# Performance work log

Measured on AMD Instinct MI355X. Metric: run time of the kernel, lower is better.

Reference implementation:

```python
import jax, jax.numpy as jnp
import numpy as np

B = 8
SEQ = 8192
D_MODEL = 256
D_STATE = 64
D_CONV = 4
EXPAND = 4
HEADDIM = 64
N_LAYERS = 8
D_INNER = EXPAND * D_MODEL            # 1024
NHEADS = D_INNER // HEADDIM           # 16
CONV_DIM = D_INNER + 2 * D_STATE      # 1152 (ngroups=1)
D_IN_PROJ = 2 * D_INNER + 2 * D_STATE + NHEADS  # 2192


def setup_inputs():
    key = jax.random.key(0)
    ks = jax.random.split(key, 16)
    rn = lambda k, shape, fan: jax.random.normal(k, shape, jnp.float32) / np.float32(np.sqrt(fan))
    inp = {}
    inp["x"] = jax.random.normal(ks[0], (B, 3, SEQ), jnp.float32)
    inp["conv1_w"] = rn(ks[1], (64, 3, 16), 3 * 16)
    inp["conv1_b"] = rn(ks[2], (64,), 64)
    inp["conv2_w"] = rn(ks[3], (D_MODEL, 64, 16), 64 * 16)
    inp["conv2_b"] = rn(ks[4], (D_MODEL,), D_MODEL)
    inp["in_proj_w"] = rn(ks[5], (N_LAYERS, D_IN_PROJ, D_MODEL), D_MODEL)
    inp["dw_conv_w"] = rn(ks[6], (N_LAYERS, CONV_DIM, D_CONV), D_CONV)
    inp["dw_conv_b"] = rn(ks[7], (N_LAYERS, CONV_DIM), D_CONV)
    inp["dt_bias"] = jax.random.normal(ks[8], (N_LAYERS, NHEADS), jnp.float32) * 0.5
    inp["A_log"] = jax.random.uniform(ks[9], (N_LAYERS, NHEADS), jnp.float32, 0.0, 2.0)
    inp["ssm_D"] = jnp.ones((N_LAYERS, NHEADS), jnp.float32)
    inp["rms_w"] = jnp.ones((N_LAYERS, D_INNER), jnp.float32)
    inp["out_proj_w"] = rn(ks[10], (N_LAYERS, D_MODEL, D_INNER), D_INNER)
    inp["ln_w"] = jnp.ones((D_MODEL,), jnp.float32)
    inp["ln_b"] = jnp.zeros((D_MODEL,), jnp.float32)
    inp["reg1_w"] = rn(ks[11], (128, D_MODEL), D_MODEL)
    inp["reg1_b"] = rn(ks[12], (128,), 128)
    inp["reg2_w"] = rn(ks[13], (1, 128), 128)
    inp["reg2_b"] = rn(ks[14], (1,), 128)
    return inp


def _silu(v):
    return v * jax.nn.sigmoid(v)


def _mamba2_layer(u, in_proj_w, dw_w, dw_b, dt_bias, A_log, ssm_D, rms_w, out_proj_w):
    b, l, _ = u.shape
    zxbcdt = u @ in_proj_w.T                               # (b,l,2192)
    z = zxbcdt[..., :D_INNER]
    xBC = zxbcdt[..., D_INNER:D_INNER + CONV_DIM]
    dt = jax.nn.softplus(zxbcdt[..., D_INNER + CONV_DIM:] + dt_bias)   # (b,l,h)
    # causal depthwise conv1d (kernel D_CONV), then SiLU
    pad = jnp.pad(xBC, ((0, 0), (D_CONV - 1, 0), (0, 0)))
    conv = sum(pad[:, k:k + l, :] * dw_w[:, k] for k in range(D_CONV)) + dw_b
    xBC = _silu(conv)
    xh = xBC[..., :D_INNER].reshape(b, l, NHEADS, HEADDIM)  # (b,l,h,p)
    Bm = xBC[..., D_INNER:D_INNER + D_STATE]                # (b,l,n)
    Cm = xBC[..., D_INNER + D_STATE:]                       # (b,l,n)
    dA = jnp.exp(dt * (-jnp.exp(A_log)))                    # (b,l,h)

    def step(h, inp):
        dA_t, dt_t, x_t, B_t, C_t = inp
        h = h * dA_t[:, :, None, None] + (dt_t[:, :, None] * x_t)[..., None] * B_t[:, None, None, :]
        y = jnp.einsum('bhpn,bn->bhp', h, C_t)
        return h, y

    h0 = jnp.zeros((b, NHEADS, HEADDIM, D_STATE), u.dtype)
    xs = (dA.transpose(1, 0, 2), dt.transpose(1, 0, 2),
          xh.transpose(1, 0, 2, 3), Bm.transpose(1, 0, 2), Cm.transpose(1, 0, 2))
    _, ys = jax.lax.scan(step, h0, xs)                      # (l,b,h,p)
    y = ys.transpose(1, 0, 2, 3) + ssm_D[None, None, :, None] * xh
    y = y.reshape(b, l, D_INNER)
    y = y * _silu(z)                                        # gated
    y = y * jax.lax.rsqrt(jnp.mean(y * y, axis=-1, keepdims=True) + 1e-5) * rms_w
    return y @ out_proj_w.T


def reference(x, conv1_w, conv1_b, conv2_w, conv2_b, in_proj_w, dw_conv_w, dw_conv_b,
              dt_bias, A_log, ssm_D, rms_w, out_proj_w, ln_w, ln_b,
              reg1_w, reg1_b, reg2_w, reg2_b):
    dn = ('NCH', 'OIH', 'NCH')
    h = jax.lax.conv_general_dilated(x, conv1_w, (4,), [(6, 6)], dimension_numbers=dn) + conv1_b[None, :, None]
    h = jax.nn.gelu(h, approximate=False)
    h = jax.lax.conv_general_dilated(h, conv2_w, (2,), [(7, 7)], dimension_numbers=dn) + conv2_b[None, :, None]
    h = jax.nn.gelu(h, approximate=False)
    h = h.transpose(0, 2, 1)                                # (b, 1024, d_model)
    for i in range(N_LAYERS):
        h = _mamba2_layer(h, in_proj_w[i], dw_conv_w[i], dw_conv_b[i],
                          dt_bias[i], A_log[i], ssm_D[i], rms_w[i], out_proj_w[i])
    mu = jnp.mean(h, -1, keepdims=True)
    var = jnp.mean((h - mu) ** 2, -1, keepdims=True)
    h = (h - mu) * jax.lax.rsqrt(var + 1e-5) * ln_w + ln_b  # LayerNorm
    pooled = h.mean(1)
    r = jax.nn.gelu(pooled @ reg1_w.T + reg1_b, approximate=False)
    return r @ reg2_w.T + reg2_b                            # (b, 1)
```

## Files before the change

kernel.cpp:

```cpp
#include <hip/hip_runtime.h>
#include <math.h>

#define NB       8
#define SEQ      8192
#define L1OUT    2048
#define LOUT     1024
#define DMODEL   256
#define DINNER   1024
#define NHEADS   16
#define HEADDIM  64
#define DSTATE   64
#define CONVDIM  1152
#define DINPROJ  2192
#define NPADIN   2304
#define NLAYERS  8
#define NCHUNK   16
#define Q        64

typedef _Float16 f16;
typedef __attribute__((ext_vector_type(8))) _Float16 f16x8;
typedef __attribute__((ext_vector_type(4))) _Float16 f16x4;
typedef __attribute__((ext_vector_type(4))) float    f32x4;

__device__ __forceinline__ float gelu_f(float v) {
    return 0.5f * v * (1.0f + erff(v * 0.70710678118654752f));
}
__device__ __forceinline__ float silu_f(float v) {
    return v * __builtin_amdgcn_rcpf(1.0f + __expf(-v));
}

__device__ __forceinline__ void gload16(const void* g, void* l) {
    __builtin_amdgcn_global_load_lds(
        (const __attribute__((address_space(1))) unsigned int*)g,
        (__attribute__((address_space(3))) unsigned int*)l, 16, 0, 0);
}

__global__ __launch_bounds__(256) void k_cast(const float* __restrict__ in,
                                              f16* __restrict__ out, int n) {
    int i = blockIdx.x * 256 + threadIdx.x;
    if (i < n) out[i] = (f16)in[i];
}

__global__ __launch_bounds__(256) void k_cast_inproj(const float* __restrict__ w,
                                                     f16* __restrict__ out) {
    int idx = blockIdx.x * 256 + threadIdx.x;
    int c = idx & 255;
    int r = (idx >> 8) % NPADIN;
    int l = idx / (NPADIN * 256);
    float v = (r < DINPROJ) ? w[((size_t)l * DINPROJ + r) * 256 + c] : 0.f;
    out[idx] = (f16)v;
}

__global__ __launch_bounds__(256) void k_conv1(const float* __restrict__ x,
                                               const float* __restrict__ w,
                                               const float* __restrict__ bias,
                                               f16* __restrict__ out) {
    int idx = blockIdx.x * 256 + threadIdx.x;
    int t  = idx & (L1OUT - 1);
    int co = (idx >> 11) & 63;
    int b  = idx >> 17;
    float s = bias[co];
#pragma unroll
    for (int ci = 0; ci < 3; ++ci) {
        const float* xp = x + ((size_t)b * 3 + ci) * SEQ;
        const float* wp = w + (co * 3 + ci) * 16;
#pragma unroll
        for (int k = 0; k < 16; ++k) {
            int pos = t * 4 + k - 6;
            if (pos >= 0 && pos < SEQ) s = fmaf(xp[pos], wp[k], s);
        }
    }
    out[idx] = (f16)gelu_f(s);
}

__global__ __launch_bounds__(256) void k_im2col(const f16* __restrict__ h1,
                                                f16* __restrict__ A) {
    int idx = blockIdx.x * 256 + threadIdx.x;
    int col = idx & 1023;
    int row = idx >> 10;
    int t = row & (LOUT - 1);
    int b = row >> 10;
    int ci = col >> 4, k = col & 15;
    int pos = t * 2 + k - 7;
    f16 v = (f16)0.f;
    if (pos >= 0 && pos < L1OUT) v = h1[((size_t)b * 64 + ci) * L1OUT + pos];
    A[idx] = v;
}

template<int BM, int EPI>
__global__ __launch_bounds__(256) void k_hgemm(const f16* __restrict__ A,
                                               const f16* __restrict__ Bw,
                                               f16* __restrict__ Ch,
                                               int M, int N, int K,
                                               const float* __restrict__ bias,
                                               const float* __restrict__ dt_bias,
                                               const float* __restrict__ A_log,
                                               float* __restrict__ dadt) {
    constexpr int MI = BM / 32;
    __shared__ f16 As[BM * 32];
    __shared__ f16 Bs[128 * 32];
    int tid  = threadIdx.x;
    int lane = tid & 63, wid = tid >> 6;
    int wm = wid >> 1, wn = wid & 1;
    int row0 = blockIdx.y * BM, col0 = blockIdx.x * 128;
    int lr = lane & 15, kb = lane >> 4;

    f32x4 acc[MI][4];
#pragma unroll
    for (int mi = 0; mi < MI; ++mi)
#pragma unroll
        for (int ni = 0; ni < 4; ++ni)
            acc[mi][ni] = (f32x4){0.f, 0.f, 0.f, 0.f};

    int srow = tid >> 2;
    int scol = (tid & 3) * 8;

    for (int k0 = 0; k0 < K; k0 += 32) {
        __syncthreads();
#pragma unroll
        for (int is = 0; is < BM / 64; ++is)
            gload16(A + (size_t)(row0 + is * 64 + srow) * K + k0 + scol,
                    &As[is * 2048 + wid * 512]);
#pragma unroll
        for (int is = 0; is < 2; ++is)
            gload16(Bw + (size_t)(col0 + is * 64 + srow) * K + k0 + scol,
                    &Bs[is * 2048 + wid * 512]);
        __syncthreads();

        f16x8 a[MI], b[4];
#pragma unroll
        for (int mi = 0; mi < MI; ++mi)
            a[mi] = *reinterpret_cast<const f16x8*>(
                &As[(wm * (BM / 2) + mi * 16 + lr) * 32 + kb * 8]);
#pragma unroll
        for (int ni = 0; ni < 4; ++ni)
            b[ni] = *reinterpret_cast<const f16x8*>(
                &Bs[(wn * 64 + ni * 16 + lr) * 32 + kb * 8]);
#pragma unroll
        for (int mi = 0; mi < MI; ++mi)
#pragma unroll
            for (int ni = 0; ni < 4; ++ni)
                acc[mi][ni] = __builtin_amdgcn_mfma_f32_16x16x32_f16(
                    a[mi], b[ni], acc[mi][ni], 0, 0, 0);
    }

#pragma unroll
    for (int mi = 0; mi < MI; ++mi)
#pragma unroll
        for (int ni = 0; ni < 4; ++ni) {
            int ccol = col0 + wn * 64 + ni * 16 + lr;
            if (ccol < N) {
                int rbase = row0 + wm * (BM / 2) + mi * 16 + kb * 4;
                f32x4 v = acc[mi][ni];
#pragma unroll
                for (int r = 0; r < 4; ++r) {
                    float val = v[r];
                    if (EPI == 1) val = gelu_f(val + bias[ccol]);
                    Ch[(size_t)(rbase + r) * N + ccol] = (f16)val;
                    if (EPI == 2 && ccol >= DINNER + CONVDIM) {
                        int hh = ccol - (DINNER + CONVDIM);
                        float raw = val + dt_bias[hh];
                        float dtv = (raw > 20.f) ? raw : log1pf(__expf(raw));
                        float lda = -__expf(A_log[hh]) * dtv;
                        *(float2*)&dadt[(size_t)(rbase + r) * 32 + hh * 2] =
                            make_float2(lda, dtv);
                    }
                }
            }
        }
}

__global__ __launch_bounds__(256) void k_ssd1(const f16* __restrict__ zx16,
                                              const float* __restrict__ dadt,
                                              const float* __restrict__ dw_w,
                                              const float* __restrict__ dw_b,
                                              const float* __restrict__ ssmD,
                                              f16* __restrict__ y1,
                                              f16* __restrict__ Sbuf16,
                                              float* __restrict__ Abuf,
                                              f16* __restrict__ C16) {
    __shared__ f16 Bs[64][72];
    __shared__ f16 Cs[64][72];
    __shared__ float GT[64][68];
    __shared__ f16 Mw[4][64][72];
    __shared__ float2 LaDt[4][64];

    int tid = threadIdx.x, lane = tid & 63, wid = tid >> 6;
    int bid = blockIdx.x;
    int hq = bid & 3, c = (bid >> 2) & 15, b = bid >> 6;
    int h = hq * 4 + wid;
    int lr = lane & 15, kb = lane >> 4;
    f16* Xs = &Mw[0][0][0];

    {
        int sg = tid % 48;
        int ts = tid / 48;
        if (ts < 4) {
            int xc;
            if (sg < 32)      xc = hq * 256 + sg * 8;
            else if (sg < 40) xc = 1024 + (sg - 32) * 8;
            else              xc = 1088 + (sg - 40) * 8;
            int zc = 1024 + xc;
            float4 wv[8];
            float  bv[8];
#pragma unroll
            for (int j = 0; j < 8; ++j) {
                wv[j] = *(const float4*)&dw_w[(xc + j) * 4];
                bv[j] = dw_b[xc + j];
            }
            int l0 = c * 64 + ts * 16;
            const f16* zrow = zx16 + ((size_t)(b * 1024 + l0)) * DINPROJ + zc;
            f16x8 r0, r1, r2, r3;
            f16x8 zz;
#pragma unroll
            for (int j = 0; j < 8; ++j) zz[j] = (f16)0.f;
            r0 = (l0 >= 3) ? *(const f16x8*)(zrow - 3 * DINPROJ) : zz;
            r1 = (l0 >= 2) ? *(const f16x8*)(zrow - 2 * DINPROJ) : zz;
            r2 = (l0 >= 1) ? *(const f16x8*)(zrow - 1 * DINPROJ) : zz;
#pragma unroll
            for (int t = 0; t < 16; ++t) {
                r3 = *(const f16x8*)(zrow + t * DINPROJ);
                f16x8 o;
#pragma unroll
                for (int j = 0; j < 8; ++j) {
                    float s = bv[j];
                    s = fmaf((float)r0[j], wv[j].x, s);
                    s = fmaf((float)r1[j], wv[j].y, s);
                    s = fmaf((float)r2[j], wv[j].z, s);
                    s = fmaf((float)r3[j], wv[j].w, s);
                    o[j] = (f16)silu_f(s);
                }
                int row = ts * 16 + t;
                if (sg < 32) {
                    f16x4 o0 = {o[0], o[1], o[2], o[3]};
                    f16x4 o1 = {o[4], o[5], o[6], o[7]};
                    *(f16x4*)&Xs[row * 260 + sg * 8]     = o0;
                    *(f16x4*)&Xs[row * 260 + sg * 8 + 4] = o1;
                } else if (sg < 40) {
                    *(f16x8*)&Bs[row][(sg - 32) * 8] = o;
                } else {
                    *(f16x8*)&Cs[row][(sg - 40) * 8] = o;
                }
                r0 = r1; r1 = r2; r2 = r3;
            }
        }
    }

    float2 ad = *(const float2*)&dadt[((size_t)(b * 1024 + c * 64 + lane) * 16 + h) * 2];
    float La = ad.x;
#pragma unroll
    for (int o = 1; o < 64; o <<= 1) {
        float v = __shfl_up(La, o);
        if (lane >= o) La += v;
    }
    float dt_own = ad.y;
    float La63 = __shfl(La, 63);
    float w_own = __expf(La63 - La) * dt_own;
    LaDt[wid][lane] = make_float2(La, dt_own);
    float Dh = ssmD[h];
    __syncthreads();

    if (hq == 0) {
        f16* cp = C16 + (((size_t)(b * 16 + c)) << 12);
#pragma unroll
        for (int it = 0; it < 2; ++it) {
            int cid = it * 256 + tid;
            int row = cid >> 3, off = (cid & 7) * 8;
            *(f16x8*)&cp[row * 64 + off] = *(const f16x8*)&Cs[row][off];
        }
    }

    f16x8 xfrag[4][2];
#pragma unroll
    for (int pi = 0; pi < 4; ++pi)
#pragma unroll
        for (int ks = 0; ks < 2; ++ks) {
            f16x8 v;
#pragma unroll
            for (int j = 0; j < 8; ++j)
                v[j] = Xs[(ks * 32 + kb * 8 + j) * 260 + wid * 64 + pi * 16 + lr];
            xfrag[pi][ks] = v;
        }

    {
        int tq = wid & 1, sq = wid >> 1;
        f32x4 g[2][2];
#pragma unroll
        for (int i = 0; i < 2; ++i)
#pragma unroll
            for (int j = 0; j < 2; ++j) g[i][j] = (f32x4){0.f, 0.f, 0.f, 0.f};
#pragma unroll
        for (int ks = 0; ks < 2; ++ks) {
            f16x8 a[2], bb[2];
#pragma unroll
            for (int ti = 0; ti < 2; ++ti)
                a[ti] = *(const f16x8*)&Cs[tq * 32 + ti * 16 + lr][ks * 32 + kb * 8];
#pragma unroll
            for (int si = 0; si < 2; ++si)
                bb[si] = *(const f16x8*)&Bs[sq * 32 + si * 16 + lr][ks * 32 + kb * 8];
#pragma unroll
            for (int ti = 0; ti < 2; ++ti)
#pragma unroll
                for (int si = 0; si < 2; ++si)
                    g[ti][si] = __builtin_amdgcn_mfma_f32_16x16x32_f16(
                        a[ti], bb[si], g[ti][si], 0, 0, 0);
        }
#pragma unroll
        for (int ti = 0; ti < 2; ++ti)
#pragma unroll
            for (int si = 0; si < 2; ++si)
#pragma unroll
                for (int r = 0; r < 4; ++r)
                    GT[sq * 32 + si * 16 + lr][tq * 32 + ti * 16 + kb * 4 + r] = g[ti][si][r];
    }
    __syncthreads();

    {
        f16x8 brow[8];
#pragma unroll
        for (int i = 0; i < 8; ++i) brow[i] = *(const f16x8*)&Bs[lane][i * 8];
#pragma unroll
        for (int i = 0; i < 8; ++i)
#pragma unroll
            for (int j = 0; j < 8; ++j)
                Mw[wid][i * 8 + j][lane] = (f16)((float)brow[i][j] * w_own);
    }
    __builtin_amdgcn_wave_barrier();

    f16x8 sbfrag[4][2];
#pragma unroll
    for (int ni = 0; ni < 4; ++ni)
#pragma unroll
        for (int ks = 0; ks < 2; ++ks)
            sbfrag[ni][ks] = *(const f16x8*)&Mw[wid][ni * 16 + lr][ks * 32 + kb * 8];

    {
        f32x4 accS[4][4];
#pragma unroll
        for (int pi = 0; pi < 4; ++pi)
#pragma unroll
            for (int ni = 0; ni < 4; ++ni) accS[pi][ni] = (f32x4){0.f, 0.f, 0.f, 0.f};
#pragma unroll
        for (int ks = 0; ks < 2; ++ks)
#pragma unroll
            for (int pi = 0; pi < 4; ++pi)
#pragma unroll
                for (int ni = 0; ni < 4; ++ni)
                    accS[pi][ni] = __builtin_amdgcn_mfma_f32_16x16x32_f16(
                        xfrag[pi][ks], sbfrag[ni][ks], accS[pi][ni], 0, 0, 0);
        size_t sbase = ((size_t)((b * 16 + h) * 16 + c)) << 12;
#pragma unroll
        for (int pi = 0; pi < 4; ++pi)
#pragma unroll
            for (int ni = 0; ni < 4; ++ni)
#pragma unroll
                for (int r = 0; r < 4; ++r)
                    Sbuf16[sbase + (size_t)(pi * 16 + kb * 4 + r) * 64 + ni * 16 + lr] =
                        (f16)accS[pi][ni][r];
        if (lane == 0) Abuf[(b * 16 + h) * 16 + c] = __expf(La63);
    }
    __builtin_amdgcn_wave_barrier();

    {
        int t = lane;
        float la_t = La;
#pragma unroll
        for (int s8 = 0; s8 < 8; ++s8) {
            f16x8 mv;
#pragma unroll
            for (int j = 0; j < 8; ++j) {
                int s = s8 * 8 + j;
                float2 ld = LaDt[wid][s];
                float m = (s <= t) ? GT[s][t] * __expf(la_t - ld.x) * ld.y : 0.f;
                if (s == t) m += Dh;
                mv[j] = (f16)m;
            }
            *(f16x8*)&Mw[wid][t][s8 * 8] = mv;
        }
    }
    __builtin_amdgcn_wave_barrier();

    {
        f32x4 accY[4][4];
#pragma unroll
        for (int ti = 0; ti < 4; ++ti)
#pragma unroll
            for (int pi = 0; pi < 4; ++pi) accY[ti][pi] = (f32x4){0.f, 0.f, 0.f, 0.f};
#pragma unroll
        for (int ks = 0; ks < 2; ++ks) {
            f16x8 af[4];
#pragma unroll
            for (int ti = 0; ti < 4; ++ti)
                af[ti] = *(const f16x8*)&Mw[wid][ti * 16 + lr][ks * 32 + kb * 8];
#pragma unroll
            for (int ti = 0; ti < 4; ++ti)
#pragma unroll
                for (int pi = 0; pi < 4; ++pi)
                    accY[ti][pi] = __builtin_amdgcn_mfma_f32_16x16x32_f16(
                        af[ti], xfrag[pi][ks], accY[ti][pi], 0, 0, 0);
        }
        f16* yp = y1 + ((size_t)(b * 1024 + c * 64)) * 1024 + h * 64;
#pragma unroll
        for (int ti = 0; ti < 4; ++ti)
#pragma unroll
            for (int pi = 0; pi < 4; ++pi)
#pragma unroll
                for (int r = 0; r < 4; ++r)
                    yp[(size_t)(ti * 16 + kb * 4 + r) * 1024 + pi * 16 + lr] =
                        (f16)accY[ti][pi][r];
    }
}

__global__ __launch_bounds__(64) void k_hscan(const f16* __restrict__ Sbuf16,
                                              const float* __restrict__ Abuf,
                                              f16* __restrict__ H16) {
    int tid = threadIdx.x;
    int bid = blockIdx.x;
    int bh = bid >> 2, q = bid & 3;
    size_t base = (size_t)bh << 16;
    int off = q * 1024 + tid * 16;
    float Hl[16];
#pragma unroll
    for (int j = 0; j < 16; ++j) Hl[j] = 0.f;
    for (int c = 0; c < NCHUNK; ++c) {
        f16x8 o0, o1;
#pragma unroll
        for (int j = 0; j < 8; ++j) { o0[j] = (f16)Hl[j]; o1[j] = (f16)Hl[j + 8]; }
        *(f16x8*)&H16[base + (size_t)c * 4096 + off] = o0;
        *(f16x8*)&H16[base + (size_t)c * 4096 + off + 8] = o1;
        float A = Abuf[bh * 16 + c];
        f16x8 s0 = *(const f16x8*)&Sbuf16[base + (size_t)c * 4096 + off];
        f16x8 s1 = *(const f16x8*)&Sbuf16[base + (size_t)c * 4096 + off + 8];
#pragma unroll
        for (int j = 0; j < 8; ++j) {
            Hl[j]     = fmaf(Hl[j],     A, (float)s0[j]);
            Hl[j + 8] = fmaf(Hl[j + 8], A, (float)s1[j]);
        }
    }
}

__global__ __launch_bounds__(64) void k_ssd2(const f16* __restrict__ C16,
                                             const float* __restrict__ dadt,
                                             const f16* __restrict__ H16,
                                             f16* __restrict__ y2) {
    __shared__ float La64[64];
    int lane = threadIdx.x;
    int bid = blockIdx.x;
    int h = bid & 15, c = (bid >> 4) & 15, b = bid >> 8;
    int lr = lane & 15, kb = lane >> 4;

    f16x8 hfrag[4][2];
    const f16* Hh = H16 + (((size_t)((b * 16 + h) * 16 + c)) << 12);
#pragma unroll
    for (int pi = 0; pi < 4; ++pi)
#pragma unroll
        for (int ks = 0; ks < 2; ++ks)
            hfrag[pi][ks] = *(const f16x8*)(Hh + (size_t)(pi * 16 + lr) * 64 + ks * 32 + kb * 8);

    float2 ad = *(const float2*)&dadt[((size_t)(b * 1024 + c * 64 + lane) * 16 + h) * 2];
    float La = ad.x;
#pragma unroll
    for (int o = 1; o < 64; o <<= 1) {
        float v = __shfl_up(La, o);
        if (lane >= o) La += v;
    }
    La64[lane] = La;
    __syncthreads();

    const f16* cp = C16 + (((size_t)(b * 16 + c)) << 12);
    f32x4 acc[4][4];
#pragma unroll
    for (int ti = 0; ti < 4; ++ti)
#pragma unroll
        for (int pi = 0; pi < 4; ++pi) acc[ti][pi] = (f32x4){0.f, 0.f, 0.f, 0.f};
#pragma unroll
    for (int ks = 0; ks < 2; ++ks) {
        f16x8 af[4];
#pragma unroll
        for (int ti = 0; ti < 4; ++ti)
            af[ti] = *(const f16x8*)(cp + (ti * 16 + lr) * 64 + ks * 32 + kb * 8);
#pragma unroll
        for (int ti = 0; ti < 4; ++ti)
#pragma unroll
            for (int pi = 0; pi < 4; ++pi)
                acc[ti][pi] = __builtin_amdgcn_mfma_f32_16x16x32_f16(
                    af[ti], hfrag[pi][ks], acc[ti][pi], 0, 0, 0);
    }
    f16* yp = y2 + ((size_t)(b * 1024 + c * 64)) * 1024 + h * 64;
#pragma unroll
    for (int ti = 0; ti < 4; ++ti)
#pragma unroll
        for (int r = 0; r < 4; ++r) {
            int t = ti * 16 + kb * 4 + r;
            float sc = __expf(La64[t]);
#pragma unroll
            for (int pi = 0; pi < 4; ++pi)
                yp[(size_t)t * 1024 + pi * 16 + lr] = (f16)(sc * acc[ti][pi][r]);
        }
}

__global__ __launch_bounds__(256) void k_gate(const f16* __restrict__ zx16,
                                              const float* __restrict__ rmsw,
                                              const f16* __restrict__ y1,
                                              const f16* __restrict__ y2,
                                              f16* __restrict__ ygate) {
    __shared__ float sh[4];
    int bl = blockIdx.x, tid = threadIdx.x;
    int c = tid * 4;
    f16x4 y1v = *reinterpret_cast<const f16x4*>(&y1[(size_t)bl * DINNER + c]);
    f16x4 y2v = *reinterpret_cast<const f16x4*>(&y2[(size_t)bl * DINNER + c]);
    f16x4 z4  = *reinterpret_cast<const f16x4*>(&zx16[(size_t)bl * DINPROJ + c]);
    float v[4];
    float ss = 0.f;
#pragma unroll
    for (int j = 0; j < 4; ++j) {
        v[j] = ((float)y1v[j] + (float)y2v[j]) * silu_f((float)z4[j]);
        ss += v[j] * v[j];
    }
    int lane = tid & 63, wid = tid >> 6;
#pragma unroll
    for (int o = 32; o > 0; o >>= 1) ss += __shfl_down(ss, o, 64);
    if (lane == 0) sh[wid] = ss;
    __syncthreads();
    float total = sh[0] + sh[1] + sh[2] + sh[3];
    float r = rsqrtf(total * (1.f / DINNER) + 1e-5f);
    f16x4 o4;
    o4.x = (f16)(v[0] * r * rmsw[c + 0]);
    o4.y = (f16)(v[1] * r * rmsw[c + 1]);
    o4.z = (f16)(v[2] * r * rmsw[c + 2]);
    o4.w = (f16)(v[3] * r * rmsw[c + 3]);
    *reinterpret_cast<f16x4*>(&ygate[(size_t)bl * DINNER + c]) = o4;
}

__global__ __launch_bounds__(256) void k_lnpool(const f16* __restrict__ h,
                                                const float* __restrict__ lnw,
                                                const float* __restrict__ lnb,
                                                float* __restrict__ pooled) {
    __shared__ float pl[4][256];
    int bid = blockIdx.x;
    int b = bid >> 5, seg = bid & 31;
    int tid = threadIdx.x, lane = tid & 63, w = tid >> 6;
    int c4 = lane * 4;
    float4 lw = *(const float4*)&lnw[c4];
    float4 lb = *(const float4*)&lnb[c4];
    float acc0 = 0.f, acc1 = 0.f, acc2 = 0.f, acc3 = 0.f;
    const f16* hb = h + ((size_t)b * 1024 + seg * 32 + w * 8) * DMODEL;
#pragma unroll
    for (int i = 0; i < 8; ++i) {
        f16x4 hv = *(const f16x4*)(hb + (size_t)i * DMODEL + c4);
        float vx = (float)hv.x, vy = (float)hv.y, vz = (float)hv.z, vw = (float)hv.w;
        float s1 = vx + vy + vz + vw;
        float s2 = vx * vx + vy * vy + vz * vz + vw * vw;
#pragma unroll
        for (int o = 32; o > 0; o >>= 1) {
            s1 += __shfl_xor(s1, o);
            s2 += __shfl_xor(s2, o);
        }
        float mu = s1 * (1.f / DMODEL);
        float var = s2 * (1.f / DMODEL) - mu * mu;
        float rr = rsqrtf(var + 1e-5f);
        acc0 += (vx - mu) * rr * lw.x + lb.x;
        acc1 += (vy - mu) * rr * lw.y + lb.y;
        acc2 += (vz - mu) * rr * lw.z + lb.z;
        acc3 += (vw - mu) * rr * lw.w + lb.w;
    }
    pl[w][c4 + 0] = acc0; pl[w][c4 + 1] = acc1;
    pl[w][c4 + 2] = acc2; pl[w][c4 + 3] = acc3;
    __syncthreads();
    float tot = pl[0][tid] + pl[1][tid] + pl[2][tid] + pl[3][tid];
    atomicAdd(&pooled[b * DMODEL + tid], tot * (1.f / LOUT));
}

__global__ void k_zero(float* __restrict__ p, int n) {
    int i = blockIdx.x * 256 + threadIdx.x;
    if (i < n) p[i] = 0.f;
}

__global__ __launch_bounds__(128) void k_head(const float* __restrict__ pooled,
                                              const float* __restrict__ w1,
                                              const float* __restrict__ b1,
                                              const float* __restrict__ w2,
                                              const float* __restrict__ b2,
                                              float* __restrict__ out) {
    __shared__ float red[2];
    int b = blockIdx.x, j = threadIdx.x;
    float acc = b1[j];
#pragma unroll 8
    for (int d = 0; d < DMODEL; ++d)
        acc = fmaf(pooled[b * DMODEL + d], w1[j * DMODEL + d], acc);
    float r = gelu_f(acc) * w2[j];
#pragma unroll
    for (int o = 32; o > 0; o >>= 1) r += __shfl_down(r, o, 64);
    int lane = j & 63, wid = j >> 6;
    if (lane == 0) red[wid] = r;
    __syncthreads();
    if (j == 0) out[b] = red[0] + red[1] + b2[0];
}

extern "C" void kernel_launch(void* const* d_in, const int* in_sizes, int n_in,
                              void* d_out, int out_size, void* d_ws, size_t ws_size,
                              hipStream_t stream) {
    const float* x         = (const float*)d_in[0];
    const float* conv1_w   = (const float*)d_in[1];
    const float* conv1_b   = (const float*)d_in[2];
    const float* conv2_w   = (const float*)d_in[3];
    const float* conv2_b   = (const float*)d_in[4];
    const float* in_proj_w = (const float*)d_in[5];
    const float* dw_w      = (const float*)d_in[6];
    const float* dw_b      = (const float*)d_in[7];
    const float* dt_bias   = (const float*)d_in[8];
    const float* A_log     = (const float*)d_in[9];
    const float* ssm_D     = (const float*)d_in[10];
    const float* rms_w     = (const float*)d_in[11];
    const float* out_proj_w= (const float*)d_in[12];
    const float* ln_w      = (const float*)d_in[13];
    const float* ln_b      = (const float*)d_in[14];
    const float* reg1_w    = (const float*)d_in[15];
    const float* reg1_b    = (const float*)d_in[16];
    const float* reg2_w    = (const float*)d_in[17];
    const float* reg2_b    = (const float*)d_in[18];

    float* ws = (float*)d_ws;
    size_t off = 0;
    float* dadt   = ws + off; off += (size_t)NB * LOUT * NHEADS * 2;
    float* Abuf   = ws + off; off += (size_t)NB * NHEADS * NCHUNK;
    float* pooled = ws + off; off += NB * DMODEL;

    f16* fbase = (f16*)(ws + off);
    size_t foff = 0;
    f16* c1f16  = fbase + foff; foff += (size_t)NB * 64 * L1OUT;
    f16* hbf0   = fbase + foff; foff += (size_t)NB * LOUT * DMODEL;
    f16* hbf1   = fbase + foff; foff += (size_t)NB * LOUT * DMODEL;
    f16* ygate  = fbase + foff; foff += (size_t)NB * LOUT * DINNER;
    f16* y2     = fbase + foff; foff += (size_t)NB * LOUT * DINNER;
    f16* y1     = fbase + foff; foff += (size_t)NB * LOUT * DINNER;
    f16* C16    = fbase + foff; foff += (size_t)NB * NCHUNK * 64 * 64;
    f16* zx16   = fbase + foff; foff += (size_t)NB * LOUT * DINPROJ;
    f16* Sbuf16 = fbase + foff; foff += (size_t)NB * NHEADS * NCHUNK * 4096;
    f16* w_in_h = fbase + foff; foff += (size_t)NLAYERS * NPADIN * DMODEL;
    f16* w_out_h= fbase + foff; foff += (size_t)NLAYERS * DMODEL * DINNER;
    f16* w_c2_h = fbase + foff; foff += (size_t)DMODEL * 1024;
    f16* H16    = ygate;
    f16* im2h   = y1;

    k_cast_inproj<<<(NLAYERS * NPADIN * 256) / 256, 256, 0, stream>>>(in_proj_w, w_in_h);
    k_cast<<<(NLAYERS * DMODEL * DINNER) / 256, 256, 0, stream>>>(
        out_proj_w, w_out_h, NLAYERS * DMODEL * DINNER);
    k_cast<<<(DMODEL * 1024) / 256, 256, 0, stream>>>(conv2_w, w_c2_h, DMODEL * 1024);

    k_conv1<<<(NB * 64 * L1OUT) / 256, 256, 0, stream>>>(x, conv1_w, conv1_b, c1f16);
    k_im2col<<<(NB * LOUT * 1024) / 256, 256, 0, stream>>>(c1f16, im2h);
    {
        dim3 g(256 / 128, 8192 / 64);
        k_hgemm<64, 1><<<g, 256, 0, stream>>>(im2h, w_c2_h, hbf0,
                                              8192, 256, 1024, conv2_b,
                                              nullptr, nullptr, nullptr);
    }

    f16* hcur = hbf0;
    f16* hnxt = hbf1;
    for (int i = 0; i < NLAYERS; ++i) {
        {
            dim3 g(NPADIN / 128, 8192 / 128);
            k_hgemm<128, 2><<<g, 256, 0, stream>>>(
                hcur, w_in_h + (size_t)i * NPADIN * DMODEL, zx16,
                8192, DINPROJ, DMODEL, nullptr,
                dt_bias + i * NHEADS, A_log + i * NHEADS, dadt);
        }
        k_ssd1<<<NB * NCHUNK * 4, 256, 0, stream>>>(
            zx16, dadt, dw_w + (size_t)i * CONVDIM * 4, dw_b + (size_t)i * CONVDIM,
            ssm_D + i * NHEADS, y1, Sbuf16, Abuf, C16);
        k_hscan<<<NB * NHEADS * 4, 64, 0, stream>>>(Sbuf16, Abuf, H16);
        k_ssd2<<<NB * NCHUNK * NHEADS, 64, 0, stream>>>(C16, dadt, H16, y2);
        k_gate<<<NB * LOUT, 256, 0, stream>>>(zx16, rms_w + (size_t)i * DINNER,
                                              y1, y2, ygate);
        {
            dim3 g(DMODEL / 128, 8192 / 64);
            k_hgemm<64, 0><<<g, 256, 0, stream>>>(
                ygate, w_out_h + (size_t)i * DMODEL * DINNER, hnxt,
                8192, DMODEL, DINNER, nullptr, nullptr, nullptr, nullptr);
        }
        f16* tmp = hcur; hcur = hnxt; hnxt = tmp;
    }

    k_zero<<<(NB * DMODEL + 255) / 256, 256, 0, stream>>>(pooled, NB * DMODEL);
    k_lnpool<<<NB * 32, 256, 0, stream>>>(hcur, ln_w, ln_b, pooled);
    k_head<<<NB, 128, 0, stream>>>(pooled, reg1_w, reg1_b, reg2_w, reg2_b, (float*)d_out);
}
```

Before: 944.4 us.

## Fuse state scan into SSD output kernel, widen GEMM K-tile, vectorize conv stages

Fuses the inter-chunk state scan with the C·H output matmul, so chunk states stay in LDS instead of going through a global buffer. The GEMM now uses a 64-wide K tile with an XOR-swizzled shared-memory layout to cut bank conflicts and halve the barrier count. conv1 computes 8 outputs per thread from register-cached inputs, and im2col writes 8-wide vectors. The pooled-output atomics and zero kernel are replaced by per-segment partial sums reduced in the head kernel. In exchange, the fused SSD kernel launches only 128 blocks with 128KB of LDS each, which can leave much of the GPU idle.

```diff
diff --git a/kernel.cpp b/kernel.cpp
--- a/kernel.cpp
+++ b/kernel.cpp
@@ -56,35 +56,67 @@
                                                const float* __restrict__ bias,
                                                f16* __restrict__ out) {
     int idx = blockIdx.x * 256 + threadIdx.x;
-    int t  = idx & (L1OUT - 1);
-    int co = (idx >> 11) & 63;
-    int b  = idx >> 17;
-    float s = bias[co];
+    int u  = idx & 255;
+    int co = (idx >> 8) & 63;
+    int b  = idx >> 14;
+    int xbase = u * 32 - 8;
+
+    float acc[8];
+#pragma unroll
+    for (int t = 0; t < 8; ++t) acc[t] = bias[co];
+
 #pragma unroll
     for (int ci = 0; ci < 3; ++ci) {
         const float* xp = x + ((size_t)b * 3 + ci) * SEQ;
+        float xb[48];
+#pragma unroll
+        for (int j = 0; j < 12; ++j) {
+            int off = xbase + j * 4;
+            float4 v;
+            if (off >= 0 && off + 3 < SEQ) {
+                v = *(const float4*)&xp[off];
+            } else {
+                v.x = (off + 0 >= 0 && off + 0 < SEQ) ? xp[off + 0] : 0.f;
+                v.y = (off + 1 >= 0 && off + 1 < SEQ) ? xp[off + 1] : 0.f;
+                v.z = (off + 2 >= 0 && off + 2 < SEQ) ? xp[off + 2] : 0.f;
+                v.w = (off + 3 >= 0 && off + 3 < SEQ) ? xp[off + 3] : 0.f;
+            }
+            xb[j * 4 + 0] = v.x; xb[j * 4 + 1] = v.y;
+            xb[j * 4 + 2] = v.z; xb[j * 4 + 3] = v.w;
+        }
         const float* wp = w + (co * 3 + ci) * 16;
-#pragma unroll
-        for (int k = 0; k < 16; ++k) {
-            int pos = t * 4 + k - 6;
-            if (pos >= 0 && pos < SEQ) s = fmaf(xp[pos], wp[k], s);
-        }
-    }
-    out[idx] = (f16)gelu_f(s);
+        float wv[16];
+#pragma unroll
+        for (int k = 0; k < 16; ++k) wv[k] = wp[k];
+#pragma unroll
+        for (int t = 0; t < 8; ++t)
+#pragma unroll
+            for (int k = 0; k < 16; ++k)
+                acc[t] = fmaf(xb[t * 4 + k + 2], wv[k], acc[t]);
+    }
+    f16x8 o;
+#pragma unroll
+    for (int t = 0; t < 8; ++t) o[t] = (f16)gelu_f(acc[t]);
+    *(f16x8*)&out[((size_t)(b * 64 + co)) * L1OUT + u * 8] = o;
 }
 
 __global__ __launch_bounds__(256) void k_im2col(const f16* __restrict__ h1,
                                                 f16* __restrict__ A) {
     int idx = blockIdx.x * 256 + threadIdx.x;
-    int col = idx & 1023;
-    int row = idx >> 10;
+    int g = idx & 127;
+    int row = idx >> 7;
     int t = row & (LOUT - 1);
     int b = row >> 10;
-    int ci = col >> 4, k = col & 15;
-    int pos = t * 2 + k - 7;
-    f16 v = (f16)0.f;
-    if (pos >= 0 && pos < L1OUT) v = h1[((size_t)b * 64 + ci) * L1OUT + pos];
-    A[idx] = v;
+    int ci = g >> 1, k0 = (g & 1) * 8;
+    int pos0 = t * 2 + k0 - 7;
+    const f16* hp = h1 + ((size_t)(b * 64 + ci)) * L1OUT;
+    f16x8 v;
+#pragma unroll
+    for (int j = 0; j < 8; ++j) {
+        int p = pos0 + j;
+        v[j] = (p >= 0 && p < L1OUT) ? hp[p] : (f16)0.f;
+    }
+    *(f16x8*)&A[(size_t)row * 1024 + g * 8] = v;
 }
 
 template<int BM, int EPI>
@@ -97,8 +129,8 @@
                                                const float* __restrict__ A_log,
                                                float* __restrict__ dadt) {
     constexpr int MI = BM / 32;
-    __shared__ f16 As[BM * 32];
-    __shared__ f16 Bs[128 * 32];
+    __shared__ f16 As[BM * 64];
+    __shared__ f16 Bs[128 * 64];
     int tid  = threadIdx.x;
     int lane = tid & 63, wid = tid >> 6;
     int wm = wid >> 1, wn = wid & 1;
@@ -112,36 +144,41 @@
         for (int ni = 0; ni < 4; ++ni)
             acc[mi][ni] = (f32x4){0.f, 0.f, 0.f, 0.f};
 
-    int srow = tid >> 2;
-    int scol = (tid & 3) * 8;
-
-    for (int k0 = 0; k0 < K; k0 += 32) {
+    int sr  = tid >> 3;
+    int scx = ((tid & 7) ^ (sr & 7)) * 8;
+    int rsw = (lr & 7) * 8;
+
+    for (int k0 = 0; k0 < K; k0 += 64) {
         __syncthreads();
 #pragma unroll
-        for (int is = 0; is < BM / 64; ++is)
-            gload16(A + (size_t)(row0 + is * 64 + srow) * K + k0 + scol,
+        for (int is = 0; is < BM / 32; ++is)
+            gload16(A + (size_t)(row0 + is * 32 + sr) * K + k0 + scx,
                     &As[is * 2048 + wid * 512]);
 #pragma unroll
-        for (int is = 0; is < 2; ++is)
-            gload16(Bw + (size_t)(col0 + is * 64 + srow) * K + k0 + scol,
+        for (int is = 0; is < 4; ++is)
+            gload16(Bw + (size_t)(col0 + is * 32 + sr) * K + k0 + scx,
                     &Bs[is * 2048 + wid * 512]);
         __syncthreads();
 
-        f16x8 a[MI], b[4];
-#pragma unroll
-        for (int mi = 0; mi < MI; ++mi)
-            a[mi] = *reinterpret_cast<const f16x8*>(
-                &As[(wm * (BM / 2) + mi * 16 + lr) * 32 + kb * 8]);
-#pragma unroll
-        for (int ni = 0; ni < 4; ++ni)
-            b[ni] = *reinterpret_cast<const f16x8*>(
-                &Bs[(wn * 64 + ni * 16 + lr) * 32 + kb * 8]);
-#pragma unroll
-        for (int mi = 0; mi < MI; ++mi)
+#pragma unroll
+        for (int ks = 0; ks < 2; ++ks) {
+            int cbase = (ks * 32 + kb * 8) ^ rsw;
+            f16x8 a[MI], b[4];
+#pragma unroll
+            for (int mi = 0; mi < MI; ++mi)
+                a[mi] = *reinterpret_cast<const f16x8*>(
+                    &As[(wm * (BM / 2) + mi * 16 + lr) * 64 + cbase]);
 #pragma unroll
             for (int ni = 0; ni < 4; ++ni)
-                acc[mi][ni] = __builtin_amdgcn_mfma_f32_16x16x32_f16(
-                    a[mi], b[ni], acc[mi][ni], 0, 0, 0);
+                b[ni] = *reinterpret_cast<const f16x8*>(
+                    &Bs[(wn * 64 + ni * 16 + lr) * 64 + cbase]);
+#pragma unroll
+            for (int mi = 0; mi < MI; ++mi)
+#pragma unroll
+                for (int ni = 0; ni < 4; ++ni)
+                    acc[mi][ni] = __builtin_amdgcn_mfma_f32_16x16x32_f16(
+                        a[mi], b[ni], acc[mi][ni], 0, 0, 0);
+        }
     }
 
 #pragma unroll
@@ -411,92 +448,100 @@
     }
 }
 
-__global__ __launch_bounds__(64) void k_hscan(const f16* __restrict__ Sbuf16,
-                                              const float* __restrict__ Abuf,
-                                              f16* __restrict__ H16) {
-    int tid = threadIdx.x;
-    int bid = blockIdx.x;
-    int bh = bid >> 2, q = bid & 3;
+__global__ __launch_bounds__(256) void k_ssd2f(const f16* __restrict__ C16,
+                                               const f16* __restrict__ Sbuf16,
+                                               const float* __restrict__ Abuf,
+                                               const float* __restrict__ dadt,
+                                               f16* __restrict__ y2) {
+    __shared__ f16 Hs[NCHUNK][4096];
+    int tid = threadIdx.x, lane = tid & 63, wv = tid >> 6;
+    int bh = blockIdx.x;
+    int h = bh & 15, b = bh >> 4;
+    int lr = lane & 15, kb = lane >> 4;
     size_t base = (size_t)bh << 16;
-    int off = q * 1024 + tid * 16;
-    float Hl[16];
-#pragma unroll
-    for (int j = 0; j < 16; ++j) Hl[j] = 0.f;
-    for (int c = 0; c < NCHUNK; ++c) {
-        f16x8 o0, o1;
-#pragma unroll
-        for (int j = 0; j < 8; ++j) { o0[j] = (f16)Hl[j]; o1[j] = (f16)Hl[j + 8]; }
-        *(f16x8*)&H16[base + (size_t)c * 4096 + off] = o0;
-        *(f16x8*)&H16[base + (size_t)c * 4096 + off + 8] = o1;
-        float A = Abuf[bh * 16 + c];
-        f16x8 s0 = *(const f16x8*)&Sbuf16[base + (size_t)c * 4096 + off];
-        f16x8 s1 = *(const f16x8*)&Sbuf16[base + (size_t)c * 4096 + off + 8];
-#pragma unroll
-        for (int j = 0; j < 8; ++j) {
-            Hl[j]     = fmaf(Hl[j],     A, (float)s0[j]);
-            Hl[j + 8] = fmaf(Hl[j + 8], A, (float)s1[j]);
-        }
-    }
-}
-
-__global__ __launch_bounds__(64) void k_ssd2(const f16* __restrict__ C16,
-                                             const float* __restrict__ dadt,
-                                             const f16* __restrict__ H16,
-                                             f16* __restrict__ y2) {
-    __shared__ float La64[64];
-    int lane = threadIdx.x;
-    int bid = blockIdx.x;
-    int h = bid & 15, c = (bid >> 4) & 15, b = bid >> 8;
-    int lr = lane & 15, kb = lane >> 4;
-
-    f16x8 hfrag[4][2];
-    const f16* Hh = H16 + (((size_t)((b * 16 + h) * 16 + c)) << 12);
-#pragma unroll
-    for (int pi = 0; pi < 4; ++pi)
-#pragma unroll
-        for (int ks = 0; ks < 2; ++ks)
-            hfrag[pi][ks] = *(const f16x8*)(Hh + (size_t)(pi * 16 + lr) * 64 + ks * 32 + kb * 8);
-
-    float2 ad = *(const float2*)&dadt[((size_t)(b * 1024 + c * 64 + lane) * 16 + h) * 2];
-    float La = ad.x;
-#pragma unroll
-    for (int o = 1; o < 64; o <<= 1) {
-        float v = __shfl_up(La, o);
-        if (lane >= o) La += v;
-    }
-    La64[lane] = La;
+
+    {
+        int off = tid * 16;
+        int row = tid >> 2;
+        int c0f = (tid & 3) * 16;
+        int sw = (row & 7) * 8;
+        int d0 = row * 64 + (c0f ^ sw);
+        int d1 = row * 64 + ((c0f + 8) ^ sw);
+        float Hl[16];
+#pragma unroll
+        for (int j = 0; j < 16; ++j) Hl[j] = 0.f;
+#pragma unroll
+        for (int c = 0; c < NCHUNK; ++c) {
+            f16x8 o0, o1;
+#pragma unroll
+            for (int j = 0; j < 8; ++j) { o0[j] = (f16)Hl[j]; o1[j] = (f16)Hl[j + 8]; }
+            *(f16x8*)&Hs[c][d0] = o0;
+            *(f16x8*)&Hs[c][d1] = o1;
+            float A = Abuf[bh * 16 + c];
+            f16x8 s0 = *(const f16x8*)&Sbuf16[base + (size_t)c * 4096 + off];
+            f16x8 s1 = *(const f16x8*)&Sbuf16[base + (size_t)c * 4096 + off + 8];
+#pragma unroll
+            for (int j = 0; j < 8; ++j) {
+                Hl[j]     = fmaf(Hl[j],     A, (float)s0[j]);
+                Hl[j + 8] = fmaf(Hl[j + 8], A, (float)s1[j]);
+            }
+        }
+    }
     __syncthreads();
 
-    const f16* cp = C16 + (((size_t)(b * 16 + c)) << 12);
-    f32x4 acc[4][4];
-#pragma unroll
-    for (int ti = 0; ti < 4; ++ti)
-#pragma unroll
-        for (int pi = 0; pi < 4; ++pi) acc[ti][pi] = (f32x4){0.f, 0.f, 0.f, 0.f};
-#pragma unroll
-    for (int ks = 0; ks < 2; ++ks) {
-        f16x8 af[4];
+    const f16* cpb = C16 + ((size_t)b << 16);
+#pragma unroll
+    for (int i = 0; i < 4; ++i) {
+        int c = wv * 4 + i;
+        float2 ad = *(const float2*)&dadt[((size_t)(b * 1024 + c * 64 + lane) * 16 + h) * 2];
+        float La = ad.x;
+#pragma unroll
+        for (int o = 1; o < 64; o <<= 1) {
+            float v = __shfl_up(La, o);
+            if (lane >= o) La += v;
+        }
+
+        f16x8 hfrag[4][2];
+#pragma unroll
+        for (int pi = 0; pi < 4; ++pi)
+#pragma unroll
+            for (int ks = 0; ks < 2; ++ks) {
+                int row = pi * 16 + lr;
+                int cf = (ks * 32 + kb * 8) ^ ((row & 7) * 8);
+                hfrag[pi][ks] = *(const f16x8*)&Hs[c][row * 64 + cf];
+            }
+
+        const f16* cp = cpb + ((size_t)c << 12);
+        f32x4 acc[4][4];
 #pragma unroll
         for (int ti = 0; ti < 4; ++ti)
-            af[ti] = *(const f16x8*)(cp + (ti * 16 + lr) * 64 + ks * 32 + kb * 8);
+#pragma unroll
+            for (int pi = 0; pi < 4; ++pi) acc[ti][pi] = (f32x4){0.f, 0.f, 0.f, 0.f};
+#pragma unroll
+        for (int ks = 0; ks < 2; ++ks) {
+            f16x8 af[4];
+#pragma unroll
+            for (int ti = 0; ti < 4; ++ti)
+                af[ti] = *(const f16x8*)(cp + (ti * 16 + lr) * 64 + ks * 32 + kb * 8);
+#pragma unroll
+            for (int ti = 0; ti < 4; ++ti)
+#pragma unroll
+                for (int pi = 0; pi < 4; ++pi)
+                    acc[ti][pi] = __builtin_amdgcn_mfma_f32_16x16x32_f16(
+                        af[ti], hfrag[pi][ks], acc[ti][pi], 0, 0, 0);
+        }
+        f16* yp = y2 + ((size_t)(b * 1024 + c * 64)) * 1024 + h * 64;
 #pragma unroll
         for (int ti = 0; ti < 4; ++ti)
 #pragma unroll
-            for (int pi = 0; pi < 4; ++pi)
-                acc[ti][pi] = __builtin_amdgcn_mfma_f32_16x16x32_f16(
-                    af[ti], hfrag[pi][ks], acc[ti][pi], 0, 0, 0);
-    }
-    f16* yp = y2 + ((size_t)(b * 1024 + c * 64)) * 1024 + h * 64;
-#pragma unroll
-    for (int ti = 0; ti < 4; ++ti)
-#pragma unroll
-        for (int r = 0; r < 4; ++r) {
-            int t = ti * 16 + kb * 4 + r;
-            float sc = __expf(La64[t]);
-#pragma unroll
-            for (int pi = 0; pi < 4; ++pi)
-                yp[(size_t)t * 1024 + pi * 16 + lr] = (f16)(sc * acc[ti][pi][r]);
-        }
+            for (int r = 0; r < 4; ++r) {
+                int t = ti * 16 + kb * 4 + r;
+                float sc = __expf(__shfl(La, t));
+#pragma unroll
+                for (int pi = 0; pi < 4; ++pi)
+                    yp[(size_t)t * 1024 + pi * 16 + lr] = (f16)(sc * acc[ti][pi][r]);
+            }
+    }
 }
 
 __global__ __launch_bounds__(256) void k_gate(const f16* __restrict__ zx16,
@@ -535,7 +580,7 @@
 __global__ __launch_bounds__(256) void k_lnpool(const f16* __restrict__ h,
                                                 const float* __restrict__ lnw,
                                                 const float* __restrict__ lnb,
-                                                float* __restrict__ pooled) {
+                                                float* __restrict__ pooledp) {
     __shared__ float pl[4][256];
     int bid = blockIdx.x;
     int b = bid >> 5, seg = bid & 31;
@@ -568,26 +613,30 @@
     pl[w][c4 + 2] = acc2; pl[w][c4 + 3] = acc3;
     __syncthreads();
     float tot = pl[0][tid] + pl[1][tid] + pl[2][tid] + pl[3][tid];
-    atomicAdd(&pooled[b * DMODEL + tid], tot * (1.f / LOUT));
-}
-
-__global__ void k_zero(float* __restrict__ p, int n) {
-    int i = blockIdx.x * 256 + threadIdx.x;
-    if (i < n) p[i] = 0.f;
-}
-
-__global__ __launch_bounds__(128) void k_head(const float* __restrict__ pooled,
+    pooledp[(size_t)(b * 32 + seg) * 256 + tid] = tot;
+}
+
+__global__ __launch_bounds__(128) void k_head(const float* __restrict__ pooledp,
                                               const float* __restrict__ w1,
                                               const float* __restrict__ b1,
                                               const float* __restrict__ w2,
                                               const float* __restrict__ b2,
                                               float* __restrict__ out) {
+    __shared__ float sp[256];
     __shared__ float red[2];
     int b = blockIdx.x, j = threadIdx.x;
+    for (int d = j; d < 256; d += 128) {
+        float s = 0.f;
+#pragma unroll
+        for (int seg = 0; seg < 32; ++seg)
+            s += pooledp[(size_t)(b * 32 + seg) * 256 + d];
+        sp[d] = s * (1.f / LOUT);
+    }
+    __syncthreads();
     float acc = b1[j];
 #pragma unroll 8
     for (int d = 0; d < DMODEL; ++d)
-        acc = fmaf(pooled[b * DMODEL + d], w1[j * DMODEL + d], acc);
+        acc = fmaf(sp[d], w1[j * DMODEL + d], acc);
     float r = gelu_f(acc) * w2[j];
 #pragma unroll
     for (int o = 32; o > 0; o >>= 1) r += __shfl_down(r, o, 64);
@@ -622,9 +671,9 @@
 
     float* ws = (float*)d_ws;
     size_t off = 0;
-    float* dadt   = ws + off; off += (size_t)NB * LOUT * NHEADS * 2;
-    float* Abuf   = ws + off; off += (size_t)NB * NHEADS * NCHUNK;
-    float* pooled = ws + off; off += NB * DMODEL;
+    float* dadt    = ws + off; off += (size_t)NB * LOUT * NHEADS * 2;
+    float* Abuf    = ws + off; off += (size_t)NB * NHEADS * NCHUNK;
+    float* pooledp = ws + off; off += (size_t)NB * 32 * 256;
 
     f16* fbase = (f16*)(ws + off);
     size_t foff = 0;
@@ -640,7 +689,6 @@
     f16* w_in_h = fbase + foff; foff += (size_t)NLAYERS * NPADIN * DMODEL;
     f16* w_out_h= fbase + foff; foff += (size_t)NLAYERS * DMODEL * DINNER;
     f16* w_c2_h = fbase + foff; foff += (size_t)DMODEL * 1024;
-    f16* H16    = ygate;
     f16* im2h   = y1;
 
     k_cast_inproj<<<(NLAYERS * NPADIN * 256) / 256, 256, 0, stream>>>(in_proj_w, w_in_h);
@@ -648,8 +696,8 @@
         out_proj_w, w_out_h, NLAYERS * DMODEL * DINNER);
     k_cast<<<(DMODEL * 1024) / 256, 256, 0, stream>>>(conv2_w, w_c2_h, DMODEL * 1024);
 
-    k_conv1<<<(NB * 64 * L1OUT) / 256, 256, 0, stream>>>(x, conv1_w, conv1_b, c1f16);
-    k_im2col<<<(NB * LOUT * 1024) / 256, 256, 0, stream>>>(c1f16, im2h);
+    k_conv1<<<(NB * 64 * 256) / 256, 256, 0, stream>>>(x, conv1_w, conv1_b, c1f16);
+    k_im2col<<<(NB * LOUT * 128) / 256, 256, 0, stream>>>(c1f16, im2h);
     {
         dim3 g(256 / 128, 8192 / 64);
         k_hgemm<64, 1><<<g, 256, 0, stream>>>(im2h, w_c2_h, hbf0,
@@ -670,8 +718,7 @@
         k_ssd1<<<NB * NCHUNK * 4, 256, 0, stream>>>(
             zx16, dadt, dw_w + (size_t)i * CONVDIM * 4, dw_b + (size_t)i * CONVDIM,
             ssm_D + i * NHEADS, y1, Sbuf16, Abuf, C16);
-        k_hscan<<<NB * NHEADS * 4, 64, 0, stream>>>(Sbuf16, Abuf, H16);
-        k_ssd2<<<NB * NCHUNK * NHEADS, 64, 0, stream>>>(C16, dadt, H16, y2);
+        k_ssd2f<<<NB * NHEADS, 256, 0, stream>>>(C16, Sbuf16, Abuf, dadt, y2);
         k_gate<<<NB * LOUT, 256, 0, stream>>>(zx16, rms_w + (size_t)i * DINNER,
                                               y1, y2, ygate);
         {
@@ -683,7 +730,6 @@
         f16* tmp = hcur; hcur = hnxt; hnxt = tmp;
     }
 
-    k_zero<<<(NB * DMODEL + 255) / 256, 256, 0, stream>>>(pooled, NB * DMODEL);
-    k_lnpool<<<NB * 32, 256, 0, stream>>>(hcur, ln_w, ln_b, pooled);
-    k_head<<<NB, 128, 0, stream>>>(pooled, reg1_w, reg1_b, reg2_w, reg2_b, (float*)d_out);
-}
+    k_lnpool<<<NB * 32, 256, 0, stream>>>(hcur, ln_w, ln_b, pooledp);
+    k_head<<<NB, 128, 0, stream>>>(pooledp, reg1_w, reg1_b, reg2_w, reg2_b, (float*)d_out);
+}
```

Measured after the change: 875.9 us. 7.3% less time.
